# Optimization experiments

Measured on AMD Instinct MI355X. Metric: run time of the kernel, lower is better.

The kernel has to match this reference:

```python
import jax, jax.numpy as jnp
import numpy as np

B, S, H, V = 4, 2048, 768, 32000
HID = 100          # self.hidden_size
N_LABELS = 3
LN2 = 0.6931471805599453


def setup_inputs() -> dict:
    key = jax.random.key(0)
    ks = jax.random.split(key, 10)
    return {
        "input_ids": jax.random.randint(ks[0], (B, S), 0, V),
        "attention_mask": jnp.ones((B, S), jnp.float32),
        "sentiment": jax.random.normal(ks[1], (B, 3), jnp.float32),
        "hidden_states": jax.random.normal(ks[2], (B, S, H), jnp.float32),
        "lm_logits": jax.random.normal(ks[3], (B, S, V), jnp.float32),
        "W_ih": jax.random.normal(ks[4], (4 * HID, H + 1), jnp.float32) * 0.05,
        "W_hh": jax.random.normal(ks[5], (4 * HID, HID), jnp.float32) * 0.05,
        "b_ih": jax.random.normal(ks[6], (4 * HID,), jnp.float32) * 0.05,
        "b_hh": jax.random.normal(ks[7], (4 * HID,), jnp.float32) * 0.05,
        "cls_W": jax.random.normal(ks[8], (N_LABELS, HID + 3), jnp.float32) * 0.05,
        "cls_b": jax.random.normal(ks[9], (N_LABELS,), jnp.float32) * 0.05,
    }


def _lstm_last(x, W_ih, W_hh, b_ih, b_hh):
    # x: [B,S,D] -> last hidden state [B,HID]; PyTorch gate order i,f,g,o
    b, hid = x.shape[0], W_hh.shape[1]
    x_proj = jnp.einsum('bsd,gd->bsg', x, W_ih) + b_ih + b_hh  # [B,S,4H]

    def step(carry, xt):
        h, c = carry
        gates = xt + h @ W_hh.T
        i, f, g, o = jnp.split(gates, 4, axis=-1)
        c = jax.nn.sigmoid(f) * c + jax.nn.sigmoid(i) * jnp.tanh(g)
        h = jax.nn.sigmoid(o) * jnp.tanh(c)
        return (h, c), None

    h0 = jnp.zeros((b, hid), x.dtype)
    (hT, _), _ = jax.lax.scan(step, (h0, h0), jnp.swapaxes(x_proj, 0, 1))
    return hT


def reference(input_ids, attention_mask, sentiment, hidden_states, lm_logits,
              W_ih, W_hh, b_ih, b_hh, cls_W, cls_b):
    # surprisal: -log2(softmax(logits)[input_ids]) * mask, detached
    log_p = jax.nn.log_softmax(lm_logits, axis=-1)                       # [B,S,V]
    lp = jnp.take_along_axis(log_p, input_ids[..., None], axis=2)[..., 0]  # [B,S]
    surp = jax.lax.stop_gradient((-lp / LN2) * attention_mask)

    x = jnp.concatenate([hidden_states, surp[..., None]], axis=-1)  # [B,S,H+1]
    hT = _lstm_last(x, W_ih, W_hh, b_ih, b_hh)                      # [B,HID]
    # dropout is identity at inference
    feat = jnp.concatenate([hT, sentiment], axis=1)                 # [B,HID+3]
    return feat @ cls_W.T + cls_b                                   # [B,N_LABELS]
```

## Files before the change

### kernel.cpp

```cpp
#include <hip/hip_runtime.h>
#include <hip/hip_bf16.h>
#include <math.h>

#define B 4
#define S 2048
#define H 768
#define V 32000
#define HID 100
#define G4 400
#define M_TOT (B*S)
#define PD 2

typedef _Float16 half2_t __attribute__((ext_vector_type(2)));
typedef _Float16 half8_t __attribute__((ext_vector_type(8)));

__device__ __forceinline__ float fdot2_(half2_t a, half2_t b, float c) {
#if __has_builtin(__builtin_amdgcn_fdot2)
  return __builtin_amdgcn_fdot2(a, b, c, false);
#else
  return c + (float)a[0] * (float)b[0] + (float)a[1] * (float)b[1];
#endif
}

__device__ __forceinline__ float sigmoidf_(float x) {
  return 1.0f / (1.0f + __expf(-x));
}

__device__ __forceinline__ void lds_barrier_() {
  asm volatile("s_waitcnt lgkmcnt(0)" ::: "memory");
  __builtin_amdgcn_s_barrier();
  asm volatile("" ::: "memory");
}

#define BM 64
#define BN 64
#define BK 32
#define NTM (M_TOT / BM)
#define NTN ((G4 + BN - 1) / BN)
#define NGEMM (NTM * NTN)

__global__ __launch_bounds__(256) void fused_pre_kernel(
    const float* __restrict__ logits, const int* __restrict__ ids,
    const float* __restrict__ mask, float* __restrict__ surp,
    const float* __restrict__ A,
    const float* __restrict__ W,
    const float* __restrict__ b_ih, const float* __restrict__ b_hh,
    float* __restrict__ xproj) {
  __shared__ float smem[BK * BM + BK * BN];
  int tid = threadIdx.x;

  if (blockIdx.x < NGEMM) {
    float (*As)[BM] = (float(*)[BM])smem;
    float (*Bs)[BN] = (float(*)[BN])(smem + BK * BM);
    int bid = blockIdx.x;
    int m0 = (bid / NTN) * BM;
    int n0 = (bid % NTN) * BN;
    int tx = tid & 15, ty = tid >> 4;
    float acc[4][4] = {};
    for (int k0 = 0; k0 < H; k0 += BK) {
      #pragma unroll
      for (int l = 0; l < 2; ++l) {
        int idx = tid + l * 256;
        int row = idx >> 3;
        int kq = idx & 7;
        float4 v = *(const float4*)&A[(size_t)(m0 + row) * H + k0 + kq * 4];
        As[kq * 4 + 0][row] = v.x;
        As[kq * 4 + 1][row] = v.y;
        As[kq * 4 + 2][row] = v.z;
        As[kq * 4 + 3][row] = v.w;
      }
      #pragma unroll
      for (int l = 0; l < 8; ++l) {
        int idx = tid + l * 256;
        int n = idx >> 5;
        int kk = idx & 31;
        int gn = n0 + n;
        Bs[kk][n] = (gn < G4) ? W[(size_t)gn * (H + 1) + k0 + kk] : 0.0f;
      }
      __syncthreads();
      #pragma unroll
      for (int k = 0; k < BK; ++k) {
        float4 a = *(const float4*)&As[k][ty * 4];
        float4 bq = *(const float4*)&Bs[k][tx * 4];
        float av[4] = {a.x, a.y, a.z, a.w};
        float bv[4] = {bq.x, bq.y, bq.z, bq.w};
        #pragma unroll
        for (int i = 0; i < 4; ++i)
          #pragma unroll
          for (int j = 0; j < 4; ++j)
            acc[i][j] += av[i] * bv[j];
      }
      __syncthreads();
    }
    #pragma unroll
    for (int i = 0; i < 4; ++i) {
      int gm = m0 + ty * 4 + i;
      #pragma unroll
      for (int j = 0; j < 4; ++j) {
        int gn = n0 + tx * 4 + j;
        if (gn < G4) {
          float val = acc[i][j] + b_ih[gn] + b_hh[gn];
          int g = gn / HID, k = gn % HID;
          int pn = 4 * k + (((g & 1) << 1) | (g >> 1));
          xproj[(size_t)gm * G4 + pn] = val;
        }
      }
    }
  } else {
    int row = blockIdx.x - NGEMM;
    const float* x = logits + (size_t)row * V;
    float m = -INFINITY, s = 0.0f;
    const float4* x4 = (const float4*)x;
    for (int i = tid; i < V / 4; i += 256) {
      float4 v = x4[i];
      float mv = fmaxf(fmaxf(v.x, v.y), fmaxf(v.z, v.w));
      if (mv > m) { s *= __expf(m - mv); m = mv; }
      s += __expf(v.x - m) + __expf(v.y - m) + __expf(v.z - m) + __expf(v.w - m);
    }
    #pragma unroll
    for (int off = 32; off > 0; off >>= 1) {
      float mo = __shfl_xor(m, off);
      float so = __shfl_xor(s, off);
      float mn = fmaxf(m, mo);
      s = s * __expf(m - mn) + so * __expf(mo - mn);
      m = mn;
    }
    __shared__ float sm[4], ss[4];
    int wid = tid >> 6, lane = tid & 63;
    if (lane == 0) { sm[wid] = m; ss[wid] = s; }
    __syncthreads();
    if (tid == 0) {
      float M = sm[0], Ssum = ss[0];
      #pragma unroll
      for (int w = 1; w < 4; ++w) {
        float mo = sm[w], so = ss[w];
        float mn = fmaxf(M, mo);
        Ssum = Ssum * __expf(M - mn) + so * __expf(mo - mn);
        M = mn;
      }
      float xid = x[ids[row]];
      surp[row] = (M + __logf(Ssum) - xid) * 1.4426950408889634f * mask[row];
    }
  }
}

__global__ __launch_bounds__(448) void rank1_kernel(
    const float* __restrict__ surp, const float* __restrict__ W,
    float* __restrict__ xproj) {
  int m = blockIdx.x;
  int pn = threadIdx.x;
  if (pn >= G4) return;
  int k = pn >> 2, slot = pn & 3;
  int g = ((slot & 1) << 1) | (slot >> 1);
  int gn = g * HID + k;
  float wl = W[(size_t)gn * (H + 1) + H];
  xproj[(size_t)m * G4 + pn] += surp[m] * wl;
}

#define NH2 52
__global__ __launch_bounds__(256, 1) void lstm_kernel(
    const float* __restrict__ xproj,
    const float* __restrict__ W_hh,
    const float* __restrict__ sent,
    const float* __restrict__ cls_W,
    const float* __restrict__ cls_b,
    float* __restrict__ out) {
  int b = blockIdx.x;
  int tid = threadIdx.x;
  __shared__ __align__(16) _Float16 hb0[2 * NH2];
  __shared__ __align__(16) _Float16 hb1[2 * NH2];

  bool active = tid < 200;
  int q = active ? tid : 199;
  int k = q >> 1;
  bool odd = (q & 1) != 0;
  int rA = odd ? (HID + k) : k;
  int rB = odd ? (3 * HID + k) : (2 * HID + k);

  half2_t wA[NH2], wB[NH2];
  {
    const float* pA = W_hh + (size_t)rA * HID;
    const float* pB = W_hh + (size_t)rB * HID;
    #pragma unroll
    for (int j = 0; j < 50; ++j) {
      wA[j] = half2_t{(_Float16)pA[2 * j], (_Float16)pA[2 * j + 1]};
      wB[j] = half2_t{(_Float16)pB[2 * j], (_Float16)pB[2 * j + 1]};
    }
    #pragma unroll
    for (int j = 50; j < NH2; ++j) { wA[j] = half2_t{0, 0}; wB[j] = half2_t{0, 0}; }
  }

  float c_reg = 0.0f;
  if (tid < 2 * NH2) { hb0[tid] = (_Float16)0; hb1[tid] = (_Float16)0; }
  __syncthreads();

  const float* xp = xproj + (size_t)b * S * G4;
  float2 xr[PD];
  #pragma unroll
  for (int d = 0; d < PD; ++d)
    xr[d] = ((const float2*)(xp + (size_t)d * G4))[q];

  #pragma unroll 2
  for (int t = 0; t < S; ++t) {
    int slot = t & (PD - 1);
    const half8_t* hr = (t & 1) ? (const half8_t*)hb0 : (const half8_t*)hb1;
    _Float16* hw = (t & 1) ? hb1 : hb0;

    float2 xv = xr[slot];
    {
      int tp = (t + PD < S) ? (t + PD) : (S - 1);
      xr[slot] = ((const float2*)(xp + (size_t)tp * G4))[q];
    }

    float a0 = 0.f, a1 = 0.f, b0 = 0.f, b1 = 0.f;
    #pragma unroll
    for (int j = 0; j < 13; ++j) {
      half8_t hv = hr[j];
      half2_t h0 = {hv[0], hv[1]}, h1 = {hv[2], hv[3]};
      half2_t h2 = {hv[4], hv[5]}, h3 = {hv[6], hv[7]};
      a0 = fdot2_(wA[4 * j + 0], h0, a0);
      b0 = fdot2_(wB[4 * j + 0], h0, b0);
      a1 = fdot2_(wA[4 * j + 1], h1, a1);
      b1 = fdot2_(wB[4 * j + 1], h1, b1);
      a0 = fdot2_(wA[4 * j + 2], h2, a0);
      b0 = fdot2_(wB[4 * j + 2], h2, b0);
      a1 = fdot2_(wA[4 * j + 3], h3, a1);
      b1 = fdot2_(wB[4 * j + 3], h3, b1);
    }
    float aA = a0 + a1 + xv.x;
    float aB = b0 + b1 + xv.y;

    float vA = sigmoidf_(aA);
    float sB = sigmoidf_(odd ? aB : 2.0f * aB);
    float vB = odd ? sB : (2.0f * sB - 1.0f);

    float f_n = __shfl_xor(vA, 1);
    float o_n = __shfl_xor(vB, 1);

    c_reg = f_n * c_reg + vA * vB;
    float tc = 2.0f * sigmoidf_(2.0f * c_reg) - 1.0f;
    float h = o_n * tc;
    if (active && !odd) hw[k] = (_Float16)h;

    lds_barrier_();
  }

  if (tid < 3) {
    float acc = cls_b[tid];
    const float* cw = cls_W + tid * (HID + 3);
    #pragma unroll
    for (int j = 0; j < HID; ++j) acc += cw[j] * (float)hb1[j];
    #pragma unroll
    for (int k2 = 0; k2 < 3; ++k2) acc += cw[HID + k2] * sent[b * 3 + k2];
    out[b * 3 + tid] = acc;
  }
}

extern "C" void kernel_launch(void* const* d_in, const int* in_sizes, int n_in,
                              void* d_out, int out_size, void* d_ws, size_t ws_size,
                              hipStream_t stream) {
  const int*   input_ids = (const int*)d_in[0];
  const float* mask      = (const float*)d_in[1];
  const float* sent      = (const float*)d_in[2];
  const float* hs        = (const float*)d_in[3];
  const float* logits    = (const float*)d_in[4];
  const float* W_ih      = (const float*)d_in[5];
  const float* W_hh      = (const float*)d_in[6];
  const float* b_ih      = (const float*)d_in[7];
  const float* b_hh      = (const float*)d_in[8];
  const float* cls_W     = (const float*)d_in[9];
  const float* cls_b     = (const float*)d_in[10];
  float* out = (float*)d_out;

  float* surp  = (float*)d_ws;
  float* xproj = surp + M_TOT;

  fused_pre_kernel<<<NGEMM + M_TOT, 256, 0, stream>>>(
      logits, input_ids, mask, surp, hs, W_ih, b_ih, b_hh, xproj);
  rank1_kernel<<<M_TOT, 448, 0, stream>>>(surp, W_ih, xproj);
  lstm_kernel<<<B, 256, 0, stream>>>(xproj, W_hh, sent, cls_W, cls_b, out);
}
```

Baseline: 1.419 ms.

## Fold surprisal rank-1 term into LSTM loop and interleave GEMM/softmax blocks

Removes the separate rank1 kernel that read and rewrote the whole xproj buffer, instead prefetching surprisal per timestep in the LSTM loop and adding surp*W_ih[:,H] there. It also regroups the fused pre-kernel grid so each group of 71 blocks holds the 7 GEMM tiles for one 64-row M slice plus 64 softmax rows, mixing compute-bound and bandwidth-bound blocks. This drops one launch and one full pass over xproj, at the cost of an extra load and FMA per step on the serial LSTM critical path.

```diff
diff --git a/kernel.cpp b/kernel.cpp
--- a/kernel.cpp
+++ b/kernel.cpp
@@ -38,6 +38,7 @@
 #define NTM (M_TOT / BM)
 #define NTN ((G4 + BN - 1) / BN)
 #define NGEMM (NTM * NTN)
+#define GRP 71
 
 __global__ __launch_bounds__(256) void fused_pre_kernel(
     const float* __restrict__ logits, const int* __restrict__ ids,
@@ -48,13 +49,14 @@
     float* __restrict__ xproj) {
   __shared__ float smem[BK * BM + BK * BN];
   int tid = threadIdx.x;
-
-  if (blockIdx.x < NGEMM) {
+  int grp = blockIdx.x / GRP;
+  int sub = blockIdx.x % GRP;
+
+  if (sub < NTN) {
     float (*As)[BM] = (float(*)[BM])smem;
     float (*Bs)[BN] = (float(*)[BN])(smem + BK * BM);
-    int bid = blockIdx.x;
-    int m0 = (bid / NTN) * BM;
-    int n0 = (bid % NTN) * BN;
+    int m0 = grp * BM;
+    int n0 = sub * BN;
     int tx = tid & 15, ty = tid >> 4;
     float acc[4][4] = {};
     for (int k0 = 0; k0 < H; k0 += BK) {
@@ -107,7 +109,7 @@
       }
     }
   } else {
-    int row = blockIdx.x - NGEMM;
+    int row = grp * 64 + (sub - NTN);
     const float* x = logits + (size_t)row * V;
     float m = -INFINITY, s = 0.0f;
     const float4* x4 = (const float4*)x;
@@ -125,7 +127,8 @@
       s = s * __expf(m - mn) + so * __expf(mo - mn);
       m = mn;
     }
-    __shared__ float sm[4], ss[4];
+    float* sm = smem;
+    float* ss = smem + 4;
     int wid = tid >> 6, lane = tid & 63;
     if (lane == 0) { sm[wid] = m; ss[wid] = s; }
     __syncthreads();
@@ -144,22 +147,11 @@
   }
 }
 
-__global__ __launch_bounds__(448) void rank1_kernel(
-    const float* __restrict__ surp, const float* __restrict__ W,
-    float* __restrict__ xproj) {
-  int m = blockIdx.x;
-  int pn = threadIdx.x;
-  if (pn >= G4) return;
-  int k = pn >> 2, slot = pn & 3;
-  int g = ((slot & 1) << 1) | (slot >> 1);
-  int gn = g * HID + k;
-  float wl = W[(size_t)gn * (H + 1) + H];
-  xproj[(size_t)m * G4 + pn] += surp[m] * wl;
-}
-
 #define NH2 52
 __global__ __launch_bounds__(256, 1) void lstm_kernel(
     const float* __restrict__ xproj,
+    const float* __restrict__ surp,
+    const float* __restrict__ W_ih,
     const float* __restrict__ W_hh,
     const float* __restrict__ sent,
     const float* __restrict__ cls_W,
@@ -178,6 +170,7 @@
   int rB = odd ? (3 * HID + k) : (2 * HID + k);
 
   half2_t wA[NH2], wB[NH2];
+  float wlA, wlB;
   {
     const float* pA = W_hh + (size_t)rA * HID;
     const float* pB = W_hh + (size_t)rB * HID;
@@ -188,6 +181,8 @@
     }
     #pragma unroll
     for (int j = 50; j < NH2; ++j) { wA[j] = half2_t{0, 0}; wB[j] = half2_t{0, 0}; }
+    wlA = W_ih[(size_t)rA * (H + 1) + H];
+    wlB = W_ih[(size_t)rB * (H + 1) + H];
   }
 
   float c_reg = 0.0f;
@@ -195,10 +190,14 @@
   __syncthreads();
 
   const float* xp = xproj + (size_t)b * S * G4;
+  const float* sp = surp + (size_t)b * S;
   float2 xr[PD];
+  float sr[PD];
   #pragma unroll
-  for (int d = 0; d < PD; ++d)
+  for (int d = 0; d < PD; ++d) {
     xr[d] = ((const float2*)(xp + (size_t)d * G4))[q];
+    sr[d] = sp[d];
+  }
 
   #pragma unroll 2
   for (int t = 0; t < S; ++t) {
@@ -207,9 +206,11 @@
     _Float16* hw = (t & 1) ? hb1 : hb0;
 
     float2 xv = xr[slot];
+    float sv = sr[slot];
     {
       int tp = (t + PD < S) ? (t + PD) : (S - 1);
       xr[slot] = ((const float2*)(xp + (size_t)tp * G4))[q];
+      sr[slot] = sp[tp];
     }
 
     float a0 = 0.f, a1 = 0.f, b0 = 0.f, b1 = 0.f;
@@ -227,8 +228,8 @@
       a1 = fdot2_(wA[4 * j + 3], h3, a1);
       b1 = fdot2_(wB[4 * j + 3], h3, b1);
     }
-    float aA = a0 + a1 + xv.x;
-    float aB = b0 + b1 + xv.y;
+    float aA = a0 + a1 + xv.x + sv * wlA;
+    float aB = b0 + b1 + xv.y + sv * wlB;
 
     float vA = sigmoidf_(aA);
     float sB = sigmoidf_(odd ? aB : 2.0f * aB);
@@ -275,8 +276,8 @@
   float* surp  = (float*)d_ws;
   float* xproj = surp + M_TOT;
 
-  fused_pre_kernel<<<NGEMM + M_TOT, 256, 0, stream>>>(
+  fused_pre_kernel<<<GRP * 128, 256, 0, stream>>>(
       logits, input_ids, mask, surp, hs, W_ih, b_ih, b_hh, xproj);
-  rank1_kernel<<<M_TOT, 448, 0, stream>>>(surp, W_ih, xproj);
-  lstm_kernel<<<B, 256, 0, stream>>>(xproj, W_hh, sent, cls_W, cls_b, out);
-}
+  lstm_kernel<<<B, 256, 0, stream>>>(xproj, surp, W_ih, W_hh, sent, cls_W,
+                                     cls_b, out);
+}
```

Result: slower. 1.506 ms (+6.1%).
